# Kernel tuning notes

Measured on AMD Instinct MI355X. Metric: run time of the kernel, lower is better.

The kernel has to match this reference:

```python
import jax, jax.numpy as jnp
import numpy as np

N, M_CHE, M_VDW, B = 20000, 20, 20, 200
H, E, NODE_IN, NCONV = 128, 20, 13, 3
CHE_CUTOFF, VDW_CUTOFF = 8.0, 12.0


def setup_inputs() -> dict:
    key = jax.random.key(0)
    ks = jax.random.split(key, 16)
    s = 0.05
    inp = {}
    inp['atoms_embed'] = jax.random.normal(ks[0], (N, NODE_IN), jnp.float32)
    inp['che_nbrs_fea'] = jax.random.uniform(ks[1], (N, M_CHE), jnp.float32, 0.5, CHE_CUTOFF * 1.1)
    inp['vdw_nbrs_fea'] = jax.random.uniform(ks[2], (N, M_VDW), jnp.float32, 0.5, VDW_CUTOFF * 1.1)
    inp['che_nbrs_idx'] = jax.random.randint(ks[3], (N, M_CHE), 0, N)
    inp['vdw_nbrs_idx'] = jax.random.randint(ks[4], (N, M_VDW), 0, N)
    inp['num_atoms'] = jnp.full((B,), N // B, dtype=jnp.int32)  # 200 crystals x 100 atoms
    inp['emb_W'] = jax.random.normal(ks[5], (NODE_IN, H), jnp.float32) * s
    inp['emb_b'] = jnp.zeros((H,), jnp.float32)
    inp['che_filter_W'] = jax.random.normal(ks[6], (NCONV, E, H), jnp.float32) * s
    inp['che_filter_b'] = jnp.zeros((NCONV, H), jnp.float32)
    inp['che_fc_W'] = jax.random.normal(ks[7], (NCONV, 3 * H, 2 * H), jnp.float32) * s
    inp['che_fc_b'] = jnp.zeros((NCONV, 2 * H), jnp.float32)
    inp['vdw_filter_W'] = jax.random.normal(ks[8], (NCONV, E, H), jnp.float32) * s
    inp['vdw_filter_b'] = jnp.zeros((NCONV, H), jnp.float32)
    inp['vdw_fc_W'] = jax.random.normal(ks[9], (NCONV, 3 * H, 2 * H), jnp.float32) * s
    inp['vdw_fc_b'] = jnp.zeros((NCONV, 2 * H), jnp.float32)
    inp['fc1_W'] = jax.random.normal(ks[10], (H, H), jnp.float32) * s
    inp['fc1_b'] = jnp.zeros((H,), jnp.float32)
    inp['out_W'] = jax.random.normal(ks[11], (H, 1), jnp.float32) * s
    inp['out_b'] = jnp.zeros((1,), jnp.float32)
    return inp


def _rbf(d, cutoff):
    # sinc-like radial basis with cosine envelope; zero beyond cutoff
    k = jnp.arange(1, E + 1, dtype=d.dtype)  # [E]
    de = d[..., None]  # [N, M, 1]
    r = jnp.where(de < cutoff, jnp.sin(de * k * (jnp.pi / cutoff)) / de, jnp.zeros((), d.dtype))
    env = 0.5 * (jnp.cos(jnp.pi * d / cutoff) + 1.0)
    return r * env[..., None]  # [N, M, E]


def _conv_half(nodes, rbf_e, idx, fW, fb, gW, gb):
    n, m = idx.shape
    edges = rbf_e @ fW + fb  # [N, M, H]
    self_fea = jnp.broadcast_to(nodes[:, None, :], (n, m, nodes.shape[1]))
    total = jnp.concatenate([self_fea, edges, nodes[idx]], axis=2)  # [N, M, 3H]
    gated = total @ gW + gb  # [N, M, 2H]
    filt, core = jnp.split(gated, 2, axis=2)
    return jnp.sum(jax.nn.sigmoid(filt) * jax.nn.softplus(core), axis=1)  # [N, H]


def reference(atoms_embed, che_nbrs_fea, che_nbrs_idx, vdw_nbrs_fea, vdw_nbrs_idx,
              num_atoms, emb_W, emb_b, che_filter_W, che_filter_b, che_fc_W, che_fc_b,
              vdw_filter_W, vdw_filter_b, vdw_fc_W, vdw_fc_b, fc1_W, fc1_b, out_W, out_b):
    nodes = atoms_embed @ emb_W + emb_b  # [N, H]
    che_rbf = _rbf(che_nbrs_fea, CHE_CUTOFF)
    vdw_rbf = _rbf(vdw_nbrs_fea, VDW_CUTOFF)
    for i in range(NCONV):
        che = _conv_half(nodes, che_rbf, che_nbrs_idx, che_filter_W[i], che_filter_b[i], che_fc_W[i], che_fc_b[i])
        vdw = _conv_half(nodes, vdw_rbf, vdw_nbrs_idx, vdw_filter_W[i], vdw_filter_b[i], vdw_fc_W[i], vdw_fc_b[i])
        nodes = jax.nn.softplus(nodes + che + vdw)
    # per-crystal mean pooling from contiguous atom ranges given by num_atoms
    ends = jnp.cumsum(num_atoms)
    seg = jnp.searchsorted(ends, jnp.arange(nodes.shape[0]), side='right')
    sums = jax.ops.segment_sum(nodes, seg, num_segments=B)
    crys = sums / num_atoms[:, None].astype(nodes.dtype)  # [B, H]
    crys = jax.nn.softplus(jax.nn.softplus(crys) @ fc1_W + fc1_b)
    predict = (crys @ out_W + out_b)[:, 0]  # [B]
    return predict
```

## Files before the change

### kernel.cpp

```cpp
#include <hip/hip_runtime.h>
#include <hip/hip_bf16.h>
#include <math.h>

#define NN 20000
#define MM 20
#define EE 20
#define HH 128
#define BB 200
#define NCONV 3
#define CHE_CUT 8.0f
#define VDW_CUT 12.0f
#define PI_F 3.14159265358979323846f
#define LOG2E_F 1.44269504088896340736f
#define LN2_F 0.69314718055994530942f

typedef __fp16 half2_t __attribute__((ext_vector_type(2)));
typedef __fp16 half4_t __attribute__((ext_vector_type(4)));
typedef _Float16 f16x8 __attribute__((ext_vector_type(8)));
typedef float f32x4 __attribute__((ext_vector_type(4)));

__device__ __forceinline__ float exp2_(float x) {
#if __has_builtin(__builtin_amdgcn_exp2f)
    return __builtin_amdgcn_exp2f(x);
#else
    return exp2f(x);
#endif
}
__device__ __forceinline__ float log2_(float x) {
#if __has_builtin(__builtin_amdgcn_logf)
    return __builtin_amdgcn_logf(x);
#else
    return log2f(x);
#endif
}
__device__ __forceinline__ float rcp_(float x) {
#if __has_builtin(__builtin_amdgcn_rcpf)
    return __builtin_amdgcn_rcpf(x);
#else
    return 1.f / x;
#endif
}
__device__ __forceinline__ float med3_(float a, float b, float c) {
#if __has_builtin(__builtin_amdgcn_fmed3f)
    return __builtin_amdgcn_fmed3f(a, b, c);
#else
    return fminf(a, fmaxf(b, c));
#endif
}
__device__ __forceinline__ float sin_rev_(float rev) {
#if __has_builtin(__builtin_amdgcn_sinf)
    return __builtin_amdgcn_sinf(rev);
#else
    return sinf(rev * 6.28318530717958647693f);
#endif
}
__device__ __forceinline__ float cos_rev_(float rev) {
#if __has_builtin(__builtin_amdgcn_cosf)
    return __builtin_amdgcn_cosf(rev);
#else
    return cosf(rev * 6.28318530717958647693f);
#endif
}
__device__ __forceinline__ float sp_(float x) {
    return (x > 15.f) ? x : LN2_F * log2_(1.f + exp2_(x * LOG2E_F));
}
__device__ __forceinline__ float fdot2_(half2_t a, half2_t b, float c) {
#if __has_builtin(__builtin_amdgcn_fdot2)
    return __builtin_amdgcn_fdot2(a, b, c, false);
#else
    return (float)a.x * (float)b.x + (float)a.y * (float)b.y + c;
#endif
}

__global__ void prep_bias(const float* __restrict__ cfb, const float* __restrict__ cgW,
                          const float* __restrict__ cgb,
                          const float* __restrict__ vfb, const float* __restrict__ vgW,
                          const float* __restrict__ vgb, float* __restrict__ bc) {
    int half = blockIdx.y;
    int l = blockIdx.z;
    int j = threadIdx.x;
    const float* fb = half ? vfb : cfb;
    const float* gW = half ? vgW : cgW;
    const float* gb = half ? vgb : cgb;
    const float* gWe = gW + ((size_t)l * 384 + 128) * 256;
    const float* brow = fb + (size_t)l * HH;
    float acc = gb[(size_t)l * 256 + j];
    for (int k = 0; k < HH; ++k) acc = fmaf(brow[k], gWe[k * 256 + j], acc);
    bc[((size_t)l * 2 + half) * 256 + j] = acc * LOG2E_F;
}

__global__ void prep_bwc(const float* __restrict__ cfW, const float* __restrict__ cgW,
                         const float* __restrict__ vfW, const float* __restrict__ vgW,
                         _Float16* __restrict__ bwc) {
    int nt = blockIdx.x;
    int half = blockIdx.y;
    int l = blockIdx.z;
    int tid = threadIdx.x;
    int k = tid >> 4, nc = tid & 15;
    int t = (nt & 7) * 16 + nc;
    int gcol = (nt >> 3) * 128 + t;
    const float* fW = half ? vfW : cfW;
    const float* gW = half ? vgW : cgW;
    const float* gWe = gW + ((size_t)l * 384 + 128) * 256;
    float val = 0.f;
    if (k < EE) {
        const float* frow = fW + ((size_t)l * EE + k) * HH;
        for (int kk = 0; kk < HH; ++kk) val = fmaf(frow[kk], gWe[kk * 256 + gcol], val);
        val *= LOG2E_F;
    }
    bwc[(((size_t)(l * 2 + half) * 16 + nt) * 64 + (k >> 3) * 16 + nc) * 8 + (k & 7)] = (_Float16)val;
}

__global__ void prep_bpk(const float* __restrict__ cgW, const float* __restrict__ vgW,
                         _Float16* __restrict__ bpk) {
    int i = blockIdx.x * 256 + threadIdx.x;
    if (i >= NCONV * 128 * 1024) return;
    int l = i >> 17;
    int rem = i & 131071;
    int k = rem >> 10;
    int c = rem & 1023;
    int half = (c >> 8) & 1;
    const float* src = half ? vgW : cgW;
    int grow = l * 384 + ((c < 512) ? k : 256 + k);
    float val = src[(size_t)grow * 256 + (c & 255)] * LOG2E_F;
    int nt = c >> 4, nc = c & 15;
    int s = k >> 5, kq = (k >> 3) & 3, j = k & 7;
    bpk[(size_t)l * 131072 + (((size_t)nt * 4 + s) * 64 + kq * 16 + nc) * 8 + j] = (_Float16)val;
}

__global__ void embed_kernel(const float* __restrict__ atoms, const float* __restrict__ W,
                             const float* __restrict__ bias, float* __restrict__ nodes,
                             _Float16* __restrict__ nodes_h) {
    int n = blockIdx.x, t = threadIdx.x;
    const float* arow = atoms + (size_t)n * 13;
    float acc = bias[t];
    #pragma unroll
    for (int k = 0; k < 13; ++k) acc = fmaf(arow[k], W[k * HH + t], acc);
    nodes[(size_t)n * HH + t] = acc;
    nodes_h[(size_t)n * HH + t] = (_Float16)acc;
}

__global__ void rbf_kernel(const float* __restrict__ che_fea, const float* __restrict__ vdw_fea,
                           _Float16* __restrict__ rfrag) {
    int i = blockIdx.x * blockDim.x + threadIdx.x;
    if (i >= 2 * NN * MM) return;
    bool isv = i >= NN * MM;
    int rem = isv ? i - NN * MM : i;
    int n = rem / MM, m = rem % MM;
    float d = isv ? vdw_fea[rem] : che_fea[rem];
    float cutoff = isv ? VDW_CUT : CHE_CUT;
    float rev = d * (0.5f / cutoff);
    float s1 = sin_rev_(rev);
    float c1 = cos_rev_(rev);
    float env = 0.5f * (c1 + 1.f);
    float scale = (d < cutoff) ? (env / d) : 0.f;
    float out[EE];
    float skm1 = 0.f, sk = s1;
    #pragma unroll
    for (int e = 0; e < EE; ++e) {
        out[e] = sk * scale;
        float nx = 2.f * c1 * sk - skm1;
        skm1 = sk; sk = nx;
    }
    _Float16* rf = rfrag + (size_t)(isv ? NN + n : n) * 640;
    f16x8 v0, v1, v2, v3;
    #pragma unroll
    for (int j = 0; j < 8; ++j) {
        v0[j] = (_Float16)out[j];
        v1[j] = (_Float16)out[8 + j];
        v2[j] = (j < 4) ? (_Float16)out[16 + j] : (_Float16)0.f;
        v3[j] = (_Float16)0.f;
    }
    if (m < 16) {
        _Float16* base = rf + m * 8;
        *(f16x8*)(base) = v0;
        *(f16x8*)(base + 128) = v1;
        *(f16x8*)(base + 256) = v2;
        *(f16x8*)(base + 384) = v3;
    } else {
        _Float16* base = rf + 512 + (m - 16) * 8;
        *(f16x8*)(base) = v0;
        *(f16x8*)(base + 32) = v1;
        *(f16x8*)(base + 64) = v2;
        *(f16x8*)(base + 96) = v3;
    }
}

#define GEMM_TILE(P, FB, CB)                                                     \
    do {                                                                          \
        f32x4 a0f = {0.f,0.f,0.f,0.f}, a0c = {0.f,0.f,0.f,0.f};                   \
        f32x4 a1f = {0.f,0.f,0.f,0.f}, a1c = {0.f,0.f,0.f,0.f};                   \
        _Pragma("unroll")                                                         \
        for (int s = 0; s < 4; ++s) {                                             \
            a0f = __builtin_amdgcn_mfma_f32_16x16x32_f16(af0[s], FB[s], a0f, 0, 0, 0); \
            a0c = __builtin_amdgcn_mfma_f32_16x16x32_f16(af0[s], CB[s], a0c, 0, 0, 0); \
            a1f = __builtin_amdgcn_mfma_f32_16x16x32_f16(af1[s], FB[s], a1f, 0, 0, 0); \
            a1c = __builtin_amdgcn_mfma_f32_16x16x32_f16(af1[s], CB[s], a1c, 0, 0, 0); \
        }                                                                         \
        int row_ = m0 + quad * 4;                                                 \
        int word_ = wbase + (P) * 16;                                             \
        _Pragma("unroll")                                                         \
        for (int i = 0; i < 4; ++i) {                                             \
            dst[(size_t)(row_ + i) * 256 + word_] = __builtin_amdgcn_cvt_pkrtz(a0f[i], a0c[i]); \
            dst[(size_t)(row_ + 16 + i) * 256 + word_] = __builtin_amdgcn_cvt_pkrtz(a1f[i], a1c[i]); \
        }                                                                         \
    } while (0)

__global__ __launch_bounds__(256)
void gemm_mfma(const _Float16* __restrict__ Ah, const _Float16* __restrict__ Bpk,
               half2_t* __restrict__ Spk, half2_t* __restrict__ Ypk) {
    int lane = threadIdx.x & 63;
    int wv = threadIdx.x >> 6;
    int m0 = blockIdx.x * 32;
    int la = lane & 15;
    int quad = lane >> 4;
    int k0 = quad * 8;

    f16x8 af0[4], af1[4];
    {
        const _Float16* arow = Ah + (size_t)(m0 + la) * 128 + k0;
        #pragma unroll
        for (int s = 0; s < 4; ++s) {
            af0[s] = *(const f16x8*)(arow + s * 32);
            af1[s] = *(const f16x8*)(arow + 2048 + s * 32);
        }
    }

    const f16x8* bp = (const f16x8*)Bpk;
    int ntf0 = wv * 16;
    half2_t* dst = (wv & 2) ? Ypk : Spk;
    int wbase = (wv & 1) * 128 + la;

    f16x8 fb0[4], cb0[4], fb1[4], cb1[4];
    #pragma unroll
    for (int s = 0; s < 4; ++s) {
        fb0[s] = bp[((size_t)ntf0 * 4 + s) * 64 + lane];
        cb0[s] = bp[((size_t)(ntf0 + 8) * 4 + s) * 64 + lane];
    }
    #pragma unroll
    for (int pp = 0; pp < 4; ++pp) {
        int p0 = 2 * pp, p1 = 2 * pp + 1;
        #pragma unroll
        for (int s = 0; s < 4; ++s) {
            fb1[s] = bp[((size_t)(ntf0 + p1) * 4 + s) * 64 + lane];
            cb1[s] = bp[((size_t)(ntf0 + 8 + p1) * 4 + s) * 64 + lane];
        }
        GEMM_TILE(p0, fb0, cb0);
        if (pp < 3) {
            #pragma unroll
            for (int s = 0; s < 4; ++s) {
                fb0[s] = bp[((size_t)(ntf0 + p0 + 2) * 4 + s) * 64 + lane];
                cb0[s] = bp[((size_t)(ntf0 + 10 + p0) * 4 + s) * 64 + lane];
            }
        }
        GEMM_TILE(p1, fb1, cb1);
    }
}

#define G2P 256
__global__ __launch_bounds__(256, 8)
void edge_kernel(const float* __restrict__ nodes_in, float* __restrict__ nodes_out,
                 _Float16* __restrict__ nodes_h,
                 const half2_t* __restrict__ Spk, const half2_t* __restrict__ Ypk,
                 const _Float16* __restrict__ rfrag,
                 const int* __restrict__ idx_che, const int* __restrict__ idx_vdw,
                 const _Float16* __restrict__ bwc,
                 const float* __restrict__ bC) {
    __shared__ __align__(16) unsigned char smem[20 * G2P * 4];
    half2_t* G2 = (half2_t*)smem;
    float* red = (float*)smem;
    int t = threadIdx.x;
    int lane = t & 63;
    int wv = t >> 6;
    int n = blockIdx.x;
    int h2 = t >> 7;
    int tc = t & 127;

    const int* idxp = h2 ? (idx_vdw + (size_t)n * MM) : (idx_che + (size_t)n * MM);
    int jx[MM];
    {
        const int4* ip = (const int4*)idxp;
        #pragma unroll
        for (int k = 0; k < 5; ++k) *(int4*)&jx[k * 4] = ip[k];
    }

    const half2_t* yb = Ypk + h2 * 128 + tc;
    half2_t y0 = yb[(size_t)jx[0] * 256];
    half2_t y1 = yb[(size_t)jx[1] * 256];
    half2_t y2 = yb[(size_t)jx[2] * 256];
    half2_t y3 = yb[(size_t)jx[3] * 256];

    half2_t spx = Spk[(size_t)n * 256 + h2 * 128 + tc];
    float old = (h2 == 0) ? nodes_in[(size_t)n * HH + tc] : 0.f;
    float sf = bC[h2 * 256 + tc] + (float)spx.x;
    float sc = bC[h2 * 256 + 128 + tc] + (float)spx.y;

    const half2_t ONE0 = {(__fp16)1.f, (__fp16)0.f};
    const half2_t ZERO1 = {(__fp16)0.f, (__fp16)1.f};
    int quad = lane >> 4;
    int cla = lane & 15;

    {
        int hw = wv >> 1;
        const _Float16* rf = rfrag + (size_t)(hw * NN + n) * 640;
        f16x8 a0 = *(const f16x8*)(rf + lane * 8);
        f16x8 a1 = {};
        if (cla < 4) a1 = *(const f16x8*)(rf + 512 + (quad * 4 + cla) * 8);
        const f16x8* bw = (const f16x8*)bwc + ((size_t)hw * 16) * 64;
        #pragma unroll
        for (int p = 0; p < 4; ++p) {
            int pg = (wv & 1) * 4 + p;
            f16x8 bf = bw[(size_t)pg * 64 + lane];
            f16x8 bcfr = bw[(size_t)(8 + pg) * 64 + lane];
            f32x4 g0f = {0.f, 0.f, 0.f, 0.f};
            f32x4 g0c = {0.f, 0.f, 0.f, 0.f};
            f32x4 g1f = {0.f, 0.f, 0.f, 0.f};
            f32x4 g1c = {0.f, 0.f, 0.f, 0.f};
            g0f = __builtin_amdgcn_mfma_f32_16x16x32_f16(a0, bf, g0f, 0, 0, 0);
            g0c = __builtin_amdgcn_mfma_f32_16x16x32_f16(a0, bcfr, g0c, 0, 0, 0);
            g1f = __builtin_amdgcn_mfma_f32_16x16x32_f16(a1, bf, g1f, 0, 0, 0);
            g1c = __builtin_amdgcn_mfma_f32_16x16x32_f16(a1, bcfr, g1c, 0, 0, 0);
            int col = pg * 16 + cla;
            half4_t w0;
            half2_t p0 = __builtin_amdgcn_cvt_pkrtz(g0f[0], g0c[0]);
            half2_t p1 = __builtin_amdgcn_cvt_pkrtz(g0f[1], g0c[1]);
            w0.x = p0.x; w0.y = p0.y; w0.z = p1.x; w0.w = p1.y;
            *(half4_t*)&G2[(hw * 10 + quad * 2) * G2P + col * 2] = w0;
            half4_t w1;
            half2_t p2 = __builtin_amdgcn_cvt_pkrtz(g0f[2], g0c[2]);
            half2_t p3 = __builtin_amdgcn_cvt_pkrtz(g0f[3], g0c[3]);
            w1.x = p2.x; w1.y = p2.y; w1.z = p3.x; w1.w = p3.y;
            *(half4_t*)&G2[(hw * 10 + quad * 2 + 1) * G2P + col * 2] = w1;
            if (quad == 0) {
                half4_t w2;
                half2_t q0 = __builtin_amdgcn_cvt_pkrtz(g1f[0], g1c[0]);
                half2_t q1 = __builtin_amdgcn_cvt_pkrtz(g1f[1], g1c[1]);
                w2.x = q0.x; w2.y = q0.y; w2.z = q1.x; w2.w = q1.y;
                *(half4_t*)&G2[(hw * 10 + 8) * G2P + col * 2] = w2;
                half4_t w3;
                half2_t q2 = __builtin_amdgcn_cvt_pkrtz(g1f[2], g1c[2]);
                half2_t q3 = __builtin_amdgcn_cvt_pkrtz(g1f[3], g1c[3]);
                w3.x = q2.x; w3.y = q2.y; w3.z = q3.x; w3.w = q3.y;
                *(half4_t*)&G2[(hw * 10 + 9) * G2P + col * 2] = w3;
            }
        }
    }
    __syncthreads();

    float acc = 0.f;
    const half2_t* gq = G2 + (h2 * 10) * G2P + tc * 2;
    #pragma unroll
    for (int cb = 0; cb < 5; ++cb) {
        half2_t n0 = {}, n1 = {}, n2 = {}, n3 = {};
        if (cb < 4) {
            n0 = yb[(size_t)jx[cb * 4 + 4] * 256];
            n1 = yb[(size_t)jx[cb * 4 + 5] * 256];
            n2 = yb[(size_t)jx[cb * 4 + 6] * 256];
            n3 = yb[(size_t)jx[cb * 4 + 7] * 256];
        }
        half4_t gp0 = *(const half4_t*)(gq + (size_t)(2 * cb) * G2P);
        half4_t gp1 = *(const half4_t*)(gq + (size_t)(2 * cb + 1) * G2P);
        half2_t gw0 = half2_t{gp0.x, gp0.y} + y0;
        half2_t gw1 = half2_t{gp0.z, gp0.w} + y1;
        half2_t gw2 = half2_t{gp1.x, gp1.y} + y2;
        half2_t gw3 = half2_t{gp1.z, gp1.w} + y3;
        float gf0 = fdot2_(gw0, ONE0, sf), gc0 = fdot2_(gw0, ZERO1, sc);
        float gf1 = fdot2_(gw1, ONE0, sf), gc1 = fdot2_(gw1, ZERO1, sc);
        float gf2 = fdot2_(gw2, ONE0, sf), gc2 = fdot2_(gw2, ZERO1, sc);
        float gf3 = fdot2_(gw3, ONE0, sf), gc3 = fdot2_(gw3, ZERO1, sc);
        float u0 = rcp_(1.f + exp2_(-gf0));
        float u1 = rcp_(1.f + exp2_(-gf1));
        float u2 = rcp_(1.f + exp2_(-gf2));
        float u3 = rcp_(1.f + exp2_(-gf3));
        float p0 = med3_(log2_(1.f + exp2_(gc0)), gc0, 25.f);
        float p1 = med3_(log2_(1.f + exp2_(gc1)), gc1, 25.f);
        float p2 = med3_(log2_(1.f + exp2_(gc2)), gc2, 25.f);
        float p3 = med3_(log2_(1.f + exp2_(gc3)), gc3, 25.f);
        acc = fmaf(p0, u0, acc);
        acc = fmaf(p1, u1, acc);
        acc = fmaf(p2, u2, acc);
        acc = fmaf(p3, u3, acc);
        y0 = n0; y1 = n1; y2 = n2; y3 = n3;
    }
    __syncthreads();
    if (h2) red[tc] = acc;
    __syncthreads();
    if (!h2) {
        float res = sp_(fmaf(acc + red[tc], LN2_F, old));
        nodes_out[(size_t)n * HH + tc] = res;
        nodes_h[(size_t)n * HH + tc] = (_Float16)res;
    }
}

__global__ void pool_kernel(const float* __restrict__ nodes, const int* __restrict__ num_atoms,
                            const float* __restrict__ fc1_W, const float* __restrict__ fc1_b,
                            const float* __restrict__ out_W, const float* __restrict__ out_b,
                            float* __restrict__ out) {
    __shared__ float sh[HH];
    __shared__ float red[HH];
    __shared__ int ipart[HH];
    int b = blockIdx.x, t = threadIdx.x;

    int s = 0;
    for (int i = t; i < b; i += HH) s += num_atoms[i];
    ipart[t] = s;
    __syncthreads();
    #pragma unroll
    for (int st = HH / 2; st > 0; st >>= 1) {
        if (t < st) ipart[t] += ipart[t + st];
        __syncthreads();
    }
    int start = ipart[0];
    int cnt = num_atoms[b];

    float sum = 0.f;
    for (int a = 0; a < cnt; ++a) sum += nodes[(size_t)(start + a) * HH + t];
    float mean = sum / (float)cnt;
    sh[t] = sp_(mean);
    __syncthreads();
    float o = fc1_b[t];
    #pragma unroll 4
    for (int k = 0; k < HH; ++k) o = fmaf(sh[k], fc1_W[k * HH + t], o);
    red[t] = sp_(o) * out_W[t];
    __syncthreads();
    #pragma unroll
    for (int st = HH / 2; st > 0; st >>= 1) {
        if (t < st) red[t] += red[t + st];
        __syncthreads();
    }
    if (t == 0) out[b] = red[0] + out_b[0];
}

extern "C" void kernel_launch(void* const* d_in, const int* in_sizes, int n_in,
                              void* d_out, int out_size, void* d_ws, size_t ws_size,
                              hipStream_t stream) {
    const float* atoms_embed   = (const float*)d_in[0];
    const float* che_nbrs_fea  = (const float*)d_in[1];
    const float* vdw_nbrs_fea  = (const float*)d_in[2];
    const int*   che_nbrs_idx  = (const int*)  d_in[3];
    const int*   vdw_nbrs_idx  = (const int*)  d_in[4];
    const int*   num_atoms     = (const int*)  d_in[5];
    const float* emb_W         = (const float*)d_in[6];
    const float* emb_b         = (const float*)d_in[7];
    const float* che_filter_W  = (const float*)d_in[8];
    const float* che_filter_b  = (const float*)d_in[9];
    const float* che_fc_W      = (const float*)d_in[10];
    const float* che_fc_b      = (const float*)d_in[11];
    const float* vdw_filter_W  = (const float*)d_in[12];
    const float* vdw_filter_b  = (const float*)d_in[13];
    const float* vdw_fc_W      = (const float*)d_in[14];
    const float* vdw_fc_b      = (const float*)d_in[15];
    const float* fc1_W         = (const float*)d_in[16];
    const float* fc1_b         = (const float*)d_in[17];
    const float* out_W         = (const float*)d_in[18];
    const float* out_b         = (const float*)d_in[19];
    float* out = (float*)d_out;

    float* w = (float*)d_ws;
    float* nodesA   = w;
    float* nodesB   = nodesA + (size_t)NN * HH;
    _Float16* nodes_h = (_Float16*)(nodesB + (size_t)NN * HH);
    half2_t* Spk    = (half2_t*)(nodes_h + (size_t)NN * HH);
    half2_t* Ypk    = Spk + (size_t)NN * 256;
    _Float16* rfrag = (_Float16*)(Ypk + (size_t)NN * 256);
    _Float16* bpk   = rfrag + (size_t)2 * NN * 640;
    _Float16* bwc   = bpk + (size_t)NCONV * 131072;
    float* bc       = (float*)(bwc + (size_t)NCONV * 2 * 16 * 512);

    prep_bias<<<dim3(1, 2, NCONV), 256, 0, stream>>>(
        che_filter_b, che_fc_W, che_fc_b, vdw_filter_b, vdw_fc_W, vdw_fc_b, bc);
    prep_bwc<<<dim3(16, 2, NCONV), 512, 0, stream>>>(
        che_filter_W, che_fc_W, vdw_filter_W, vdw_fc_W, bwc);
    prep_bpk<<<(NCONV * 128 * 1024 + 255) / 256, 256, 0, stream>>>(che_fc_W, vdw_fc_W, bpk);
    embed_kernel<<<NN, HH, 0, stream>>>(atoms_embed, emb_W, emb_b, nodesA, nodes_h);
    rbf_kernel<<<(2 * NN * MM + 255) / 256, 256, 0, stream>>>(
        che_nbrs_fea, vdw_nbrs_fea, rfrag);

    float* cur = nodesA;
    float* nxt = nodesB;
    for (int l = 0; l < NCONV; ++l) {
        gemm_mfma<<<NN / 32, 256, 0, stream>>>(nodes_h, bpk + (size_t)l * 131072, Spk, Ypk);
        edge_kernel<<<NN, 256, 0, stream>>>(
            cur, nxt, nodes_h, Spk, Ypk, rfrag, che_nbrs_idx, vdw_nbrs_idx,
            bwc + (size_t)l * 2 * 16 * 512, bc + (size_t)l * 512);
        float* tmp = cur; cur = nxt; nxt = tmp;
    }

    pool_kernel<<<BB, HH, 0, stream>>>(cur, num_atoms, fc1_W, fc1_b, out_W, out_b, out);
}
```

Measured before the change: 447.5 us.

## Merge prep kernels into one launch and precompute byte offsets for neighbor gathers

Folds the five setup kernels (bias, filter-weight composition, weight packing, embedding, RBF expansion) into a single kernel that dispatches on block index, removing four launches and their serialization gaps. The embedding path now handles two atoms per 256-thread block. Separately, the edge kernel precomputes 32-bit byte offsets for the gathered Ypk rows, so each load needs less address arithmetic. The merged kernel mixes very uneven work per block type, and the 32-bit offsets rely on the buffer staying under 4 GB.

```diff
diff --git a/kernel.cpp b/kernel.cpp
--- a/kernel.cpp
+++ b/kernel.cpp
@@ -72,117 +72,135 @@
 #endif
 }
 
-__global__ void prep_bias(const float* __restrict__ cfb, const float* __restrict__ cgW,
-                          const float* __restrict__ cgb,
-                          const float* __restrict__ vfb, const float* __restrict__ vgW,
-                          const float* __restrict__ vgb, float* __restrict__ bc) {
-    int half = blockIdx.y;
-    int l = blockIdx.z;
-    int j = threadIdx.x;
-    const float* fb = half ? vfb : cfb;
-    const float* gW = half ? vgW : cgW;
-    const float* gb = half ? vgb : cgb;
-    const float* gWe = gW + ((size_t)l * 384 + 128) * 256;
-    const float* brow = fb + (size_t)l * HH;
-    float acc = gb[(size_t)l * 256 + j];
-    for (int k = 0; k < HH; ++k) acc = fmaf(brow[k], gWe[k * 256 + j], acc);
-    bc[((size_t)l * 2 + half) * 256 + j] = acc * LOG2E_F;
-}
-
-__global__ void prep_bwc(const float* __restrict__ cfW, const float* __restrict__ cgW,
-                         const float* __restrict__ vfW, const float* __restrict__ vgW,
-                         _Float16* __restrict__ bwc) {
-    int nt = blockIdx.x;
-    int half = blockIdx.y;
-    int l = blockIdx.z;
+#define MB_BIAS 6
+#define MB_BWC  192
+#define MB_BPK  1536
+#define MB_EMB  10000
+#define MB_RBF  3125
+#define OFF_BWC (MB_BIAS)
+#define OFF_BPK (OFF_BWC + MB_BWC)
+#define OFF_EMB (OFF_BPK + MB_BPK)
+#define OFF_RBF (OFF_EMB + MB_EMB)
+#define MB_TOTAL (OFF_RBF + MB_RBF)
+
+__global__ __launch_bounds__(256)
+void mega_prep(const float* __restrict__ cfb, const float* __restrict__ cgW,
+               const float* __restrict__ cgb,
+               const float* __restrict__ vfb, const float* __restrict__ vgW,
+               const float* __restrict__ vgb,
+               const float* __restrict__ cfW, const float* __restrict__ vfW,
+               const float* __restrict__ atoms, const float* __restrict__ embW,
+               const float* __restrict__ embB,
+               const float* __restrict__ che_fea, const float* __restrict__ vdw_fea,
+               float* __restrict__ bc, _Float16* __restrict__ bwc,
+               _Float16* __restrict__ bpk,
+               float* __restrict__ nodes, _Float16* __restrict__ nodes_h,
+               _Float16* __restrict__ rfrag) {
+    int bi = blockIdx.x;
     int tid = threadIdx.x;
-    int k = tid >> 4, nc = tid & 15;
-    int t = (nt & 7) * 16 + nc;
-    int gcol = (nt >> 3) * 128 + t;
-    const float* fW = half ? vfW : cfW;
-    const float* gW = half ? vgW : cgW;
-    const float* gWe = gW + ((size_t)l * 384 + 128) * 256;
-    float val = 0.f;
-    if (k < EE) {
-        const float* frow = fW + ((size_t)l * EE + k) * HH;
-        for (int kk = 0; kk < HH; ++kk) val = fmaf(frow[kk], gWe[kk * 256 + gcol], val);
-        val *= LOG2E_F;
-    }
-    bwc[(((size_t)(l * 2 + half) * 16 + nt) * 64 + (k >> 3) * 16 + nc) * 8 + (k & 7)] = (_Float16)val;
-}
-
-__global__ void prep_bpk(const float* __restrict__ cgW, const float* __restrict__ vgW,
-                         _Float16* __restrict__ bpk) {
-    int i = blockIdx.x * 256 + threadIdx.x;
-    if (i >= NCONV * 128 * 1024) return;
-    int l = i >> 17;
-    int rem = i & 131071;
-    int k = rem >> 10;
-    int c = rem & 1023;
-    int half = (c >> 8) & 1;
-    const float* src = half ? vgW : cgW;
-    int grow = l * 384 + ((c < 512) ? k : 256 + k);
-    float val = src[(size_t)grow * 256 + (c & 255)] * LOG2E_F;
-    int nt = c >> 4, nc = c & 15;
-    int s = k >> 5, kq = (k >> 3) & 3, j = k & 7;
-    bpk[(size_t)l * 131072 + (((size_t)nt * 4 + s) * 64 + kq * 16 + nc) * 8 + j] = (_Float16)val;
-}
-
-__global__ void embed_kernel(const float* __restrict__ atoms, const float* __restrict__ W,
-                             const float* __restrict__ bias, float* __restrict__ nodes,
-                             _Float16* __restrict__ nodes_h) {
-    int n = blockIdx.x, t = threadIdx.x;
-    const float* arow = atoms + (size_t)n * 13;
-    float acc = bias[t];
-    #pragma unroll
-    for (int k = 0; k < 13; ++k) acc = fmaf(arow[k], W[k * HH + t], acc);
-    nodes[(size_t)n * HH + t] = acc;
-    nodes_h[(size_t)n * HH + t] = (_Float16)acc;
-}
-
-__global__ void rbf_kernel(const float* __restrict__ che_fea, const float* __restrict__ vdw_fea,
-                           _Float16* __restrict__ rfrag) {
-    int i = blockIdx.x * blockDim.x + threadIdx.x;
-    if (i >= 2 * NN * MM) return;
-    bool isv = i >= NN * MM;
-    int rem = isv ? i - NN * MM : i;
-    int n = rem / MM, m = rem % MM;
-    float d = isv ? vdw_fea[rem] : che_fea[rem];
-    float cutoff = isv ? VDW_CUT : CHE_CUT;
-    float rev = d * (0.5f / cutoff);
-    float s1 = sin_rev_(rev);
-    float c1 = cos_rev_(rev);
-    float env = 0.5f * (c1 + 1.f);
-    float scale = (d < cutoff) ? (env / d) : 0.f;
-    float out[EE];
-    float skm1 = 0.f, sk = s1;
-    #pragma unroll
-    for (int e = 0; e < EE; ++e) {
-        out[e] = sk * scale;
-        float nx = 2.f * c1 * sk - skm1;
-        skm1 = sk; sk = nx;
-    }
-    _Float16* rf = rfrag + (size_t)(isv ? NN + n : n) * 640;
-    f16x8 v0, v1, v2, v3;
-    #pragma unroll
-    for (int j = 0; j < 8; ++j) {
-        v0[j] = (_Float16)out[j];
-        v1[j] = (_Float16)out[8 + j];
-        v2[j] = (j < 4) ? (_Float16)out[16 + j] : (_Float16)0.f;
-        v3[j] = (_Float16)0.f;
-    }
-    if (m < 16) {
-        _Float16* base = rf + m * 8;
-        *(f16x8*)(base) = v0;
-        *(f16x8*)(base + 128) = v1;
-        *(f16x8*)(base + 256) = v2;
-        *(f16x8*)(base + 384) = v3;
-    } else {
-        _Float16* base = rf + 512 + (m - 16) * 8;
-        *(f16x8*)(base) = v0;
-        *(f16x8*)(base + 32) = v1;
-        *(f16x8*)(base + 64) = v2;
-        *(f16x8*)(base + 96) = v3;
+
+    if (bi < MB_BIAS) {
+        int half = bi & 1, l = bi >> 1;
+        const float* fb = half ? vfb : cfb;
+        const float* gW = half ? vgW : cgW;
+        const float* gb = half ? vgb : cgb;
+        const float* gWe = gW + ((size_t)l * 384 + 128) * 256;
+        const float* brow = fb + (size_t)l * HH;
+        float acc = gb[(size_t)l * 256 + tid];
+        for (int k = 0; k < HH; ++k) acc = fmaf(brow[k], gWe[k * 256 + tid], acc);
+        bc[((size_t)l * 2 + half) * 256 + tid] = acc * LOG2E_F;
+        return;
+    }
+    if (bi < OFF_BPK) {
+        int b2 = bi - OFF_BWC;
+        int sub = b2 & 1;
+        int nt = (b2 >> 1) & 15;
+        int half = (b2 >> 5) & 1;
+        int l = b2 >> 6;
+        int k = sub * 16 + (tid >> 4), nc = tid & 15;
+        int t = (nt & 7) * 16 + nc;
+        int gcol = (nt >> 3) * 128 + t;
+        const float* fW = half ? vfW : cfW;
+        const float* gW = half ? vgW : cgW;
+        const float* gWe = gW + ((size_t)l * 384 + 128) * 256;
+        float val = 0.f;
+        if (k < EE) {
+            const float* frow = fW + ((size_t)l * EE + k) * HH;
+            for (int kk = 0; kk < HH; ++kk) val = fmaf(frow[kk], gWe[kk * 256 + gcol], val);
+            val *= LOG2E_F;
+        }
+        bwc[(((size_t)(l * 2 + half) * 16 + nt) * 64 + (k >> 3) * 16 + nc) * 8 + (k & 7)] = (_Float16)val;
+        return;
+    }
+    if (bi < OFF_EMB) {
+        int i = (bi - OFF_BPK) * 256 + tid;
+        int l = i >> 17;
+        int rem = i & 131071;
+        int k = rem >> 10;
+        int c = rem & 1023;
+        int half = (c >> 8) & 1;
+        const float* src = half ? vgW : cgW;
+        int grow = l * 384 + ((c < 512) ? k : 256 + k);
+        float val = src[(size_t)grow * 256 + (c & 255)] * LOG2E_F;
+        int nt = c >> 4, nc = c & 15;
+        int s = k >> 5, kq = (k >> 3) & 3, j = k & 7;
+        bpk[(size_t)l * 131072 + (((size_t)nt * 4 + s) * 64 + kq * 16 + nc) * 8 + j] = (_Float16)val;
+        return;
+    }
+    if (bi < OFF_RBF) {
+        int n = (bi - OFF_EMB) * 2 + (tid >> 7);
+        int t = tid & 127;
+        const float* arow = atoms + (size_t)n * 13;
+        float acc = embB[t];
+        #pragma unroll
+        for (int k = 0; k < 13; ++k) acc = fmaf(arow[k], embW[k * HH + t], acc);
+        nodes[(size_t)n * HH + t] = acc;
+        nodes_h[(size_t)n * HH + t] = (_Float16)acc;
+        return;
+    }
+    {
+        int i = (bi - OFF_RBF) * 256 + tid;
+        bool isv = i >= NN * MM;
+        int rem = isv ? i - NN * MM : i;
+        int n = rem / MM, m = rem % MM;
+        float d = isv ? vdw_fea[rem] : che_fea[rem];
+        float cutoff = isv ? VDW_CUT : CHE_CUT;
+        float rev = d * (0.5f / cutoff);
+        float s1 = sin_rev_(rev);
+        float c1 = cos_rev_(rev);
+        float env = 0.5f * (c1 + 1.f);
+        float scale = (d < cutoff) ? (env / d) : 0.f;
+        float out[EE];
+        float skm1 = 0.f, sk = s1;
+        #pragma unroll
+        for (int e = 0; e < EE; ++e) {
+            out[e] = sk * scale;
+            float nx = 2.f * c1 * sk - skm1;
+            skm1 = sk; sk = nx;
+        }
+        _Float16* rf = rfrag + (size_t)(isv ? NN + n : n) * 640;
+        f16x8 v0, v1, v2, v3;
+        #pragma unroll
+        for (int j = 0; j < 8; ++j) {
+            v0[j] = (_Float16)out[j];
+            v1[j] = (_Float16)out[8 + j];
+            v2[j] = (j < 4) ? (_Float16)out[16 + j] : (_Float16)0.f;
+            v3[j] = (_Float16)0.f;
+        }
+        if (m < 16) {
+            _Float16* base = rf + m * 8;
+            *(f16x8*)(base) = v0;
+            *(f16x8*)(base + 128) = v1;
+            *(f16x8*)(base + 256) = v2;
+            *(f16x8*)(base + 384) = v3;
+        } else {
+            _Float16* base = rf + 512 + (m - 16) * 8;
+            *(f16x8*)(base) = v0;
+            *(f16x8*)(base + 32) = v1;
+            *(f16x8*)(base + 64) = v2;
+            *(f16x8*)(base + 96) = v3;
+        }
+        return;
     }
 }
 
@@ -277,18 +295,22 @@
     int tc = t & 127;
 
     const int* idxp = h2 ? (idx_vdw + (size_t)n * MM) : (idx_che + (size_t)n * MM);
-    int jx[MM];
+    unsigned int jo[MM];
     {
+        int jx[MM];
         const int4* ip = (const int4*)idxp;
         #pragma unroll
         for (int k = 0; k < 5; ++k) *(int4*)&jx[k * 4] = ip[k];
-    }
-
-    const half2_t* yb = Ypk + h2 * 128 + tc;
-    half2_t y0 = yb[(size_t)jx[0] * 256];
-    half2_t y1 = yb[(size_t)jx[1] * 256];
-    half2_t y2 = yb[(size_t)jx[2] * 256];
-    half2_t y3 = yb[(size_t)jx[3] * 256];
+        unsigned int tcoff = (unsigned int)(h2 * 512 + tc * 4);
+        #pragma unroll
+        for (int m = 0; m < MM; ++m) jo[m] = ((unsigned int)jx[m] << 10) + tcoff;
+    }
+    const char* ybase = (const char*)Ypk;
+
+    half2_t y0 = *(const half2_t*)(ybase + jo[0]);
+    half2_t y1 = *(const half2_t*)(ybase + jo[1]);
+    half2_t y2 = *(const half2_t*)(ybase + jo[2]);
+    half2_t y3 = *(const half2_t*)(ybase + jo[3]);
 
     half2_t spx = Spk[(size_t)n * 256 + h2 * 128 + tc];
     float old = (h2 == 0) ? nodes_in[(size_t)n * HH + tc] : 0.f;
@@ -353,10 +375,10 @@
     for (int cb = 0; cb < 5; ++cb) {
         half2_t n0 = {}, n1 = {}, n2 = {}, n3 = {};
         if (cb < 4) {
-            n0 = yb[(size_t)jx[cb * 4 + 4] * 256];
-            n1 = yb[(size_t)jx[cb * 4 + 5] * 256];
-            n2 = yb[(size_t)jx[cb * 4 + 6] * 256];
-            n3 = yb[(size_t)jx[cb * 4 + 7] * 256];
+            n0 = *(const half2_t*)(ybase + jo[cb * 4 + 4]);
+            n1 = *(const half2_t*)(ybase + jo[cb * 4 + 5]);
+            n2 = *(const half2_t*)(ybase + jo[cb * 4 + 6]);
+            n3 = *(const half2_t*)(ybase + jo[cb * 4 + 7]);
         }
         half4_t gp0 = *(const half4_t*)(gq + (size_t)(2 * cb) * G2P);
         half4_t gp1 = *(const half4_t*)(gq + (size_t)(2 * cb + 1) * G2P);
@@ -467,14 +489,11 @@
     _Float16* bwc   = bpk + (size_t)NCONV * 131072;
     float* bc       = (float*)(bwc + (size_t)NCONV * 2 * 16 * 512);
 
-    prep_bias<<<dim3(1, 2, NCONV), 256, 0, stream>>>(
-        che_filter_b, che_fc_W, che_fc_b, vdw_filter_b, vdw_fc_W, vdw_fc_b, bc);
-    prep_bwc<<<dim3(16, 2, NCONV), 512, 0, stream>>>(
-        che_filter_W, che_fc_W, vdw_filter_W, vdw_fc_W, bwc);
-    prep_bpk<<<(NCONV * 128 * 1024 + 255) / 256, 256, 0, stream>>>(che_fc_W, vdw_fc_W, bpk);
-    embed_kernel<<<NN, HH, 0, stream>>>(atoms_embed, emb_W, emb_b, nodesA, nodes_h);
-    rbf_kernel<<<(2 * NN * MM + 255) / 256, 256, 0, stream>>>(
-        che_nbrs_fea, vdw_nbrs_fea, rfrag);
+    mega_prep<<<MB_TOTAL, 256, 0, stream>>>(
+        che_filter_b, che_fc_W, che_fc_b, vdw_filter_b, vdw_fc_W, vdw_fc_b,
+        che_filter_W, vdw_filter_W,
+        atoms_embed, emb_W, emb_b, che_nbrs_fea, vdw_nbrs_fea,
+        bc, bwc, bpk, nodesA, nodes_h, rfrag);
 
     float* cur = nodesA;
     float* nxt = nodesB;
```

Measured after the change: 421.2 us (median of 2 runs). -5.9%, faster.
